# Optimization experiments

Hardware: AMD Instinct MI355X
Metric: run time of the kernel (lower is better)

## Reference

```python
import jax, jax.numpy as jnp
import numpy as np

N_NODES = 50000
N_EDGES = 1_600_000
D_IN = 128
D_HID = 128
D_OUT = 128


def _linear_init(key, out_dim, in_dim, bias=True):
    k1, k2 = jax.random.split(key)
    bound = 1.0 / np.sqrt(in_dim)
    W = jax.random.uniform(k1, (out_dim, in_dim), jnp.float32, -bound, bound)
    if bias:
        b = jax.random.uniform(k2, (out_dim,), jnp.float32, -bound, bound)
        return W, b
    return W, None


def _leconv_params(key, in_dim, out_dim):
    k1, k2, k3 = jax.random.split(key, 3)
    W1, b1 = _linear_init(k1, out_dim, in_dim, bias=True)   # lin1 (applied to x_j)
    W2, _ = _linear_init(k2, out_dim, in_dim, bias=False)   # lin2 (applied to x_i)
    W3, b3 = _linear_init(k3, out_dim, in_dim, bias=True)   # lin3 (skip on x_i)
    return W1, b1, W2, W3, b3


def setup_inputs() -> dict:
    key = jax.random.key(0)
    kx, ke, kw, k_in, k_mid, k_out = jax.random.split(key, 6)
    x = jax.random.normal(kx, (N_NODES, D_IN), jnp.float32)
    edge_index = jax.random.randint(ke, (2, N_EDGES), 0, N_NODES, dtype=jnp.int32)
    edge_weight = jax.random.uniform(kw, (N_EDGES,), jnp.float32)
    iW1, ib1, iW2, iW3, ib3 = _leconv_params(k_in, D_IN, D_HID)
    mW1, mb1, mW2, mW3, mb3 = _leconv_params(k_mid, D_HID, D_HID)
    oW1, ob1, oW2, oW3, ob3 = _leconv_params(k_out, D_HID, D_OUT)
    return {
        "x": x, "edge_index": edge_index, "edge_weight": edge_weight,
        "in_W1": iW1, "in_b1": ib1, "in_W2": iW2, "in_W3": iW3, "in_b3": ib3,
        "mid_W1": mW1, "mid_b1": mb1, "mid_W2": mW2, "mid_W3": mW3, "mid_b3": mb3,
        "out_W1": oW1, "out_b1": ob1, "out_W2": oW2, "out_W3": oW3, "out_b3": ob3,
        "number_of_layers": 4,
    }


def _leconv(h, src, dst, ew, W1, b1, W2, W3, b3):
    # out_i = sum_{j->i} e_ji * ((W1 x_j + b1) - W2 x_i) + (W3 x_i + b3)
    a = h @ W1.T + b1          # [N, F_out]
    b = h @ W2.T               # [N, F_out]
    msg = ew[:, None] * (a[src] - b[dst])              # [E, F_out]
    agg = jax.ops.segment_sum(msg, dst, num_segments=h.shape[0])
    return agg + h @ W3.T + b3


def _lrelu(x):
    return jnp.where(x >= 0, x, 0.1 * x)


def reference(x, edge_index, edge_weight,
              in_W1, in_b1, in_W2, in_W3, in_b3,
              mid_W1, mid_b1, mid_W2, mid_W3, mid_b3,
              out_W1, out_b1, out_W2, out_W3, out_b3,
              number_of_layers):
    src, dst = edge_index[0], edge_index[1]
    h = _lrelu(_leconv(x, src, dst, edge_weight, in_W1, in_b1, in_W2, in_W3, in_b3))
    for _ in range(number_of_layers - 2):  # shared inner weights, as in the torch module
        h = _lrelu(_leconv(h, src, dst, edge_weight, mid_W1, mid_b1, mid_W2, mid_W3, mid_b3))
    h = _lrelu(_leconv(h, src, dst, edge_weight, out_W1, out_b1, out_W2, out_W3, out_b3))
    return jax.nn.sigmoid(h)
```

## Files before the change

### kernel.cpp

```cpp
#include <hip/hip_runtime.h>
#include <hip/hip_fp16.h>
#include <math.h>

#define D 128
#define CSH 13
#define BSH 9
#define NB_MAX 128

typedef _Float16 f16;
typedef __attribute__((ext_vector_type(8))) _Float16 f16x8;
typedef __attribute__((ext_vector_type(4))) float f32x4;


__global__ __launch_bounds__(256) void binA_count(
    const int* __restrict__ dst, int* __restrict__ bucketCount, int E)
{
    __shared__ int hist[NB_MAX];
    int tid = threadIdx.x;
    if (tid < NB_MAX) hist[tid] = 0;
    __syncthreads();
    int base = blockIdx.x * 4096;
    for (int i = tid; i < 4096; i += 256) {
        int e = base + i;
        if (e < E) atomicAdd(&hist[dst[e] >> BSH], 1);
    }
    __syncthreads();
    if (tid < NB_MAX && hist[tid]) atomicAdd(&bucketCount[tid], hist[tid]);
}

__global__ void bucket_scan(
    const int* __restrict__ bucketCount, int* __restrict__ bucketBase,
    int* __restrict__ bucketCursor, int* __restrict__ row_off,
    int NBUC, int E, int N)
{
    if (threadIdx.x == 0 && blockIdx.x == 0) {
        int p = 0;
        for (int b = 0; b < NBUC; ++b) {
            bucketBase[b] = p; bucketCursor[b] = p; p += bucketCount[b];
        }
        bucketBase[NBUC] = p;
        row_off[N] = E;
    }
}

__global__ __launch_bounds__(256) void binA_scatter(
    const int* __restrict__ src, const int* __restrict__ dst,
    const float* __restrict__ ew, int* __restrict__ bucketCursor,
    int4* __restrict__ binned, int E)
{
    __shared__ int hist[NB_MAX], off[NB_MAX], cbase[NB_MAX];
    int tid = threadIdx.x;
    if (tid < NB_MAX) { hist[tid] = 0; off[tid] = 0; }
    __syncthreads();
    int base = blockIdx.x * 4096;
    for (int i = tid; i < 4096; i += 256) {
        int e = base + i;
        if (e < E) atomicAdd(&hist[dst[e] >> BSH], 1);
    }
    __syncthreads();
    if (tid < NB_MAX && hist[tid])
        cbase[tid] = atomicAdd(&bucketCursor[tid], hist[tid]);
    __syncthreads();
    for (int i = tid; i < 4096; i += 256) {
        int e = base + i;
        if (e < E) {
            int d = dst[e];
            int b = d >> BSH;
            int pos = cbase[b] + atomicAdd(&off[b], 1);
            binned[pos] = make_int4(src[e], __float_as_int(ew[e]), d, 0);
        }
    }
}

__global__ __launch_bounds__(1024) void binB_kernel(
    const int4* __restrict__ binned, const int* __restrict__ bucketBase,
    int2* __restrict__ edge_s, int* __restrict__ row_off,
    float* __restrict__ sdeg, int N, int nchunk)
{
    __shared__ int hist[4096];
    __shared__ int cur[4096];
    __shared__ float sdl[512];
    __shared__ int wsum[16];

    int b    = blockIdx.x;
    int tid  = threadIdx.x;
    int ebeg = bucketBase[b], eend = bucketBase[b + 1];
    int node0 = b << BSH;
    int nib   = min(512, N - node0);

    for (int i = tid; i < 4096; i += 1024) hist[i] = 0;
    for (int i = tid; i < 512; i += 1024) sdl[i] = 0.f;
    __syncthreads();

    for (int e = ebeg + tid; e < eend; e += 1024) {
        int4 ed = binned[e];
        int dl = ed.z - node0;
        int ch = ((unsigned)ed.x) >> CSH;
        atomicAdd(&hist[dl * nchunk + ch], 1);
        atomicAdd(&sdl[dl], __int_as_float(ed.y));
    }
    __syncthreads();

    int t4 = tid * 4;
    int h0 = hist[t4], h1 = hist[t4 + 1], h2 = hist[t4 + 2], h3 = hist[t4 + 3];
    int sum = h0 + h1 + h2 + h3;
    int lane = tid & 63, wid = tid >> 6;
    int x = sum;
    #pragma unroll
    for (int o = 1; o < 64; o <<= 1) { int t = __shfl_up(x, o); if (lane >= o) x += t; }
    if (lane == 63) wsum[wid] = x;
    __syncthreads();
    if (tid < 16) {
        int y = wsum[tid];
        #pragma unroll
        for (int o = 1; o < 16; o <<= 1) { int t = __shfl_up(y, o, 16); if (tid >= o) y += t; }
        wsum[tid] = y;
    }
    __syncthreads();
    int excl = (wid ? wsum[wid - 1] : 0) + x - sum;
    cur[t4] = excl; cur[t4 + 1] = excl + h0;
    cur[t4 + 2] = excl + h0 + h1; cur[t4 + 3] = excl + h0 + h1 + h2;
    __syncthreads();

    for (int dl = tid; dl < nib; dl += 1024) {
        row_off[node0 + dl] = ebeg + cur[dl * nchunk];
        sdeg[node0 + dl]    = sdl[dl];
    }
    __syncthreads();

    for (int e = ebeg + tid; e < eend; e += 1024) {
        int4 ed = binned[e];
        int dl = ed.z - node0;
        int ch = ((unsigned)ed.x) >> CSH;
        int pos = ebeg + atomicAdd(&cur[dl * nchunk + ch], 1);
        edge_s[pos] = make_int2(ed.x, ed.y);
    }
}

__global__ __launch_bounds__(256) void pack_kernel(
    const float* __restrict__ W1, const float* __restrict__ W2,
    const float* __restrict__ W3, f16* __restrict__ Wp)
{
    int idx = blockIdx.x * 256 + threadIdx.x;
    if (idx >= 6144) return;
    int lane = idx & 63;
    int t    = idx >> 6;
    int ks   = t & 3;
    int mot  = t >> 2;
    int m    = mot >> 3;
    int ot   = mot & 7;
    const float* W = (m == 0) ? W1 : (m == 1) ? W2 : W3;
    int o  = ot * 16 + (lane & 15);
    int kb = ks * 32 + (lane >> 4) * 8;
    f16x8 hi, lo;
    #pragma unroll
    for (int j = 0; j < 8; ++j) {
        float v = W[(size_t)o * D + kb + j];
        f16 hh = (f16)v;
        hi[j] = hh;
        lo[j] = (f16)(v - (float)hh);
    }
    size_t base = (size_t)ks * 24576 + (size_t)mot * 1024 + (size_t)lane * 8;
    *(f16x8*)&Wp[base]       = hi;
    *(f16x8*)&Wp[base + 512] = lo;
}

__global__ __launch_bounds__(256, 3) void gemm_kernel(
    const float* __restrict__ in, const f16* __restrict__ Wp,
    const float* __restrict__ b1, const float* __restrict__ b3,
    const float* __restrict__ sdeg, float* __restrict__ aA,
    float* __restrict__ aB, float* __restrict__ base_out, int N)
{
    __shared__ f16 Blds[24576];

    int tid  = threadIdx.x;
    int lane = tid & 63;
    int wid  = tid >> 6;
    int n0   = (blockIdx.x * 4 + wid) * 16;
    int col  = lane & 15;
    int g    = lane >> 4;
    int nrow = n0 + col;

    f32x4 acc[24];
    #pragma unroll
    for (int i = 0; i < 24; ++i) acc[i] = (f32x4){0.f, 0.f, 0.f, 0.f};

    for (int ks = 0; ks < 4; ++ks) {
        float av[8];
        if (nrow < N) {
            float4 a0 = *(const float4*)&in[(size_t)nrow * D + ks * 32 + g * 8];
            float4 a1 = *(const float4*)&in[(size_t)nrow * D + ks * 32 + g * 8 + 4];
            av[0] = a0.x; av[1] = a0.y; av[2] = a0.z; av[3] = a0.w;
            av[4] = a1.x; av[5] = a1.y; av[6] = a1.z; av[7] = a1.w;
        } else {
            #pragma unroll
            for (int j = 0; j < 8; ++j) av[j] = 0.f;
        }
        f16x8 ahi, alo;
        #pragma unroll
        for (int j = 0; j < 8; ++j) {
            f16 hh = (f16)av[j];
            ahi[j] = hh;
            alo[j] = (f16)(av[j] - (float)hh);
        }

        __syncthreads();
        {
            const f16x8* s4 = (const f16x8*)(Wp + (size_t)ks * 24576);
            f16x8* d4 = (f16x8*)Blds;
            for (int i = tid; i < 3072; i += 256) d4[i] = s4[i];
        }
        __syncthreads();

        #pragma unroll
        for (int mot = 0; mot < 24; ++mot) {
            f16x8 bhi = *(const f16x8*)&Blds[mot * 1024 + lane * 8];
            f16x8 blo = *(const f16x8*)&Blds[mot * 1024 + 512 + lane * 8];
            acc[mot] = __builtin_amdgcn_mfma_f32_16x16x32_f16(ahi, bhi, acc[mot], 0, 0, 0);
            acc[mot] = __builtin_amdgcn_mfma_f32_16x16x32_f16(alo, bhi, acc[mot], 0, 0, 0);
            acc[mot] = __builtin_amdgcn_mfma_f32_16x16x32_f16(ahi, blo, acc[mot], 0, 0, 0);
        }
    }

    #pragma unroll
    for (int ot = 0; ot < 8; ++ot) {
        int o = ot * 16 + col;
        float bi1 = b1[o];
        float bi3 = b3[o];
        float* ah = (o < 64) ? aA : aB;
        int    oh = o & 63;
        #pragma unroll
        for (int r = 0; r < 4; ++r) {
            int node = n0 + g * 4 + r;
            if (node < N) {
                float sv   = sdeg[node];
                float aval = acc[ot][r] + bi1;
                float bval = acc[16 + ot][r] + bi3 - sv * acc[8 + ot][r];
                ah[(size_t)node * 64 + oh]     = aval;
                base_out[(size_t)node * D + o] = bval;
            }
        }
    }
}


__global__ __launch_bounds__(256) void agg_kernel(
    const float* __restrict__ aH, const float* __restrict__ base,
    const int* __restrict__ row_off, const int2* __restrict__ edge_s,
    float* __restrict__ out, int N, int hofs, int last)
{
    int lane = threadIdx.x & 63;
    int node = blockIdx.x * 4 + (threadIdx.x >> 6);
    if (node >= N) return;

    float acc = base[(size_t)node * D + hofs + lane];
    int beg = row_off[node];
    int end = row_off[node + 1];

    int e = beg;
    if ((e & 1) && e < end) {
        int2 ed = edge_s[e];
        acc = fmaf(__int_as_float(ed.y), aH[(size_t)ed.x * 64 + lane], acc);
        ++e;
    }
    for (; e + 16 <= end; e += 16) {
        int4 ed[8];
        #pragma unroll
        for (int i = 0; i < 8; ++i) ed[i] = *(const int4*)&edge_s[e + i * 2];
        float v[16];
        #pragma unroll
        for (int i = 0; i < 8; ++i) {
            v[2 * i]     = aH[(size_t)ed[i].x * 64 + lane];
            v[2 * i + 1] = aH[(size_t)ed[i].z * 64 + lane];
        }
        #pragma unroll
        for (int i = 0; i < 8; ++i) {
            acc = fmaf(__int_as_float(ed[i].y), v[2 * i], acc);
            acc = fmaf(__int_as_float(ed[i].w), v[2 * i + 1], acc);
        }
    }
    for (; e + 4 <= end; e += 4) {
        int4 e0 = *(const int4*)&edge_s[e];
        int4 e1 = *(const int4*)&edge_s[e + 2];
        float v0 = aH[(size_t)e0.x * 64 + lane];
        float v1 = aH[(size_t)e0.z * 64 + lane];
        float v2 = aH[(size_t)e1.x * 64 + lane];
        float v3 = aH[(size_t)e1.z * 64 + lane];
        acc = fmaf(__int_as_float(e0.y), v0, acc);
        acc = fmaf(__int_as_float(e0.w), v1, acc);
        acc = fmaf(__int_as_float(e1.y), v2, acc);
        acc = fmaf(__int_as_float(e1.w), v3, acc);
    }
    for (; e < end; ++e) {
        int2 ed = edge_s[e];
        acc = fmaf(__int_as_float(ed.y), aH[(size_t)ed.x * 64 + lane], acc);
    }

    acc = acc >= 0.f ? acc : 0.1f * acc;
    if (last) acc = 1.f / (1.f + __expf(-acc));
    out[(size_t)node * D + hofs + lane] = acc;
}


extern "C" void kernel_launch(void* const* d_in, const int* in_sizes, int n_in,
                              void* d_out, int out_size, void* d_ws, size_t ws_size,
                              hipStream_t stream) {
    const float* x   = (const float*)d_in[0];
    const int*   ei  = (const int*)d_in[1];
    const float* ew  = (const float*)d_in[2];
    const float* iW1 = (const float*)d_in[3];
    const float* ib1 = (const float*)d_in[4];
    const float* iW2 = (const float*)d_in[5];
    const float* iW3 = (const float*)d_in[6];
    const float* ib3 = (const float*)d_in[7];
    const float* mW1 = (const float*)d_in[8];
    const float* mb1 = (const float*)d_in[9];
    const float* mW2 = (const float*)d_in[10];
    const float* mW3 = (const float*)d_in[11];
    const float* mb3 = (const float*)d_in[12];
    const float* oW1 = (const float*)d_in[13];
    const float* ob1 = (const float*)d_in[14];
    const float* oW2 = (const float*)d_in[15];
    const float* oW3 = (const float*)d_in[16];
    const float* ob3 = (const float*)d_in[17];

    int N = in_sizes[0] / D;
    int E = in_sizes[2];
    const int* src = ei;
    const int* dst = ei + E;
    int nchunk = (N + (1 << CSH) - 1) >> CSH;
    int NBUC   = (N + (1 << BSH) - 1) >> BSH;

    char* wsp = (char*)d_ws;
    size_t off = 0;
    auto alloc = [&](size_t bytes) -> void* {
        void* p = wsp + off;
        off += (bytes + 255) & ~(size_t)255;
        return p;
    };
    float* h        = (float*)alloc((size_t)N * D * 4);
    float* base     = (float*)alloc((size_t)N * D * 4);
    float* aA       = (float*)alloc((size_t)N * 64 * 4);
    float* aB       = (float*)alloc((size_t)N * 64 * 4);
    float* sdeg     = (float*)alloc((size_t)N * 4);
    int*   row_off  = (int*)alloc((size_t)(N + 1) * 4);
    int2*  edge_s   = (int2*)alloc((size_t)E * 8);
    int*   bucketCount  = (int*)alloc((size_t)(NBUC + 1) * 4);
    int*   bucketBase   = (int*)alloc((size_t)(NBUC + 1) * 4);
    int*   bucketCursor = (int*)alloc((size_t)(NBUC + 1) * 4);
    f16*   Wp       = (f16*)alloc((size_t)3 * 98304 * 2);

    int4* binned = (int4*)h;

    hipMemsetAsync(bucketCount, 0, (size_t)(NBUC + 1) * 4, stream);

    int ablocks  = (N + 3) / 4;
    int tiles    = (N + 15) / 16;
    int gblocks  = (tiles + 3) / 4;
    int abblocks = (E + 4095) / 4096;

    pack_kernel<<<24, 256, 0, stream>>>(iW1, iW2, iW3, Wp);
    pack_kernel<<<24, 256, 0, stream>>>(mW1, mW2, mW3, Wp + 98304);
    pack_kernel<<<24, 256, 0, stream>>>(oW1, oW2, oW3, Wp + 2 * 98304);

    binA_count<<<abblocks, 256, 0, stream>>>(dst, bucketCount, E);
    bucket_scan<<<1, 64, 0, stream>>>(bucketCount, bucketBase, bucketCursor,
                                      row_off, NBUC, E, N);
    binA_scatter<<<abblocks, 256, 0, stream>>>(src, dst, ew, bucketCursor,
                                               binned, E);
    binB_kernel<<<NBUC, 1024, 0, stream>>>(binned, bucketBase, edge_s,
                                           row_off, sdeg, N, nchunk);

    gemm_kernel<<<gblocks, 256, 0, stream>>>(x, Wp, ib1, ib3, sdeg, aA, aB, base, N);
    agg_kernel<<<ablocks, 256, 0, stream>>>(aA, base, row_off, edge_s, h, N, 0, 0);
    agg_kernel<<<ablocks, 256, 0, stream>>>(aB, base, row_off, edge_s, h, N, 64, 0);
    for (int l = 0; l < 2; ++l) {
        gemm_kernel<<<gblocks, 256, 0, stream>>>(h, Wp + 98304, mb1, mb3, sdeg, aA, aB, base, N);
        agg_kernel<<<ablocks, 256, 0, stream>>>(aA, base, row_off, edge_s, h, N, 0, 0);
        agg_kernel<<<ablocks, 256, 0, stream>>>(aB, base, row_off, edge_s, h, N, 64, 0);
    }
    gemm_kernel<<<gblocks, 256, 0, stream>>>(h, Wp + 2 * 98304, ob1, ob3, sdeg, aA, aB, base, N);
    agg_kernel<<<ablocks, 256, 0, stream>>>(aA, base, row_off, edge_s, (float*)d_out, N, 0, 1);
    agg_kernel<<<ablocks, 256, 0, stream>>>(aB, base, row_off, edge_s, (float*)d_out, N, 64, 1);
}
```

Measured before the change: 727.3 us.

## Make GEMM persistent with register-resident weights and merge agg halves into one launch

The GEMM kernel now runs a fixed grid of persistent blocks, and each wave keeps its slice of the packed split-f16 weights in registers. This replaces re-staging the full weight matrix through LDS for every 64-row block. Each block processes 16-row tiles, with its four waves splitting the output columns. The two aggregation launches per layer are combined into one kernel in which paired waves handle the two 64-column halves of the same node. The register-resident weights raise VGPR pressure and lower occupancy, and each input tile is now read by four waves.

Measured after the change: 679.9 us. 6.5% less time.

```diff
diff --git a/kernel.cpp b/kernel.cpp
--- a/kernel.cpp
+++ b/kernel.cpp
@@ -165,93 +165,115 @@
     *(f16x8*)&Wp[base + 512] = lo;
 }
 
-__global__ __launch_bounds__(256, 3) void gemm_kernel(
+
+__global__ __launch_bounds__(256, 2) void gemm_kernel(
     const float* __restrict__ in, const f16* __restrict__ Wp,
     const float* __restrict__ b1, const float* __restrict__ b3,
     const float* __restrict__ sdeg, float* __restrict__ aA,
-    float* __restrict__ aB, float* __restrict__ base_out, int N)
-{
-    __shared__ f16 Blds[24576];
-
+    float* __restrict__ aB, float* __restrict__ base_out,
+    int N, int ntiles, int gridb)
+{
     int tid  = threadIdx.x;
     int lane = tid & 63;
     int wid  = tid >> 6;
-    int n0   = (blockIdx.x * 4 + wid) * 16;
     int col  = lane & 15;
     int g    = lane >> 4;
-    int nrow = n0 + col;
-
-    f32x4 acc[24];
+
+    f16x8 w[3][2][4][2];
     #pragma unroll
-    for (int i = 0; i < 24; ++i) acc[i] = (f32x4){0.f, 0.f, 0.f, 0.f};
-
-    for (int ks = 0; ks < 4; ++ks) {
-        float av[8];
-        if (nrow < N) {
-            float4 a0 = *(const float4*)&in[(size_t)nrow * D + ks * 32 + g * 8];
-            float4 a1 = *(const float4*)&in[(size_t)nrow * D + ks * 32 + g * 8 + 4];
-            av[0] = a0.x; av[1] = a0.y; av[2] = a0.z; av[3] = a0.w;
-            av[4] = a1.x; av[5] = a1.y; av[6] = a1.z; av[7] = a1.w;
-        } else {
+    for (int m = 0; m < 3; ++m)
+        #pragma unroll
+        for (int oti = 0; oti < 2; ++oti) {
+            int mot = m * 8 + wid * 2 + oti;
             #pragma unroll
-            for (int j = 0; j < 8; ++j) av[j] = 0.f;
-        }
-        f16x8 ahi, alo;
-        #pragma unroll
-        for (int j = 0; j < 8; ++j) {
-            f16 hh = (f16)av[j];
-            ahi[j] = hh;
-            alo[j] = (f16)(av[j] - (float)hh);
-        }
-
-        __syncthreads();
-        {
-            const f16x8* s4 = (const f16x8*)(Wp + (size_t)ks * 24576);
-            f16x8* d4 = (f16x8*)Blds;
-            for (int i = tid; i < 3072; i += 256) d4[i] = s4[i];
-        }
-        __syncthreads();
-
-        #pragma unroll
-        for (int mot = 0; mot < 24; ++mot) {
-            f16x8 bhi = *(const f16x8*)&Blds[mot * 1024 + lane * 8];
-            f16x8 blo = *(const f16x8*)&Blds[mot * 1024 + 512 + lane * 8];
-            acc[mot] = __builtin_amdgcn_mfma_f32_16x16x32_f16(ahi, bhi, acc[mot], 0, 0, 0);
-            acc[mot] = __builtin_amdgcn_mfma_f32_16x16x32_f16(alo, bhi, acc[mot], 0, 0, 0);
-            acc[mot] = __builtin_amdgcn_mfma_f32_16x16x32_f16(ahi, blo, acc[mot], 0, 0, 0);
-        }
-    }
-
+            for (int ks = 0; ks < 4; ++ks) {
+                const f16* p = Wp + (size_t)ks * 24576 + (size_t)mot * 1024 + (size_t)lane * 8;
+                w[m][oti][ks][0] = *(const f16x8*)p;
+                w[m][oti][ks][1] = *(const f16x8*)(p + 512);
+            }
+        }
+
+    float bi1[2], bi3[2];
     #pragma unroll
-    for (int ot = 0; ot < 8; ++ot) {
-        int o = ot * 16 + col;
-        float bi1 = b1[o];
-        float bi3 = b3[o];
-        float* ah = (o < 64) ? aA : aB;
-        int    oh = o & 63;
-        #pragma unroll
-        for (int r = 0; r < 4; ++r) {
-            int node = n0 + g * 4 + r;
-            if (node < N) {
-                float sv   = sdeg[node];
-                float aval = acc[ot][r] + bi1;
-                float bval = acc[16 + ot][r] + bi3 - sv * acc[8 + ot][r];
-                ah[(size_t)node * 64 + oh]     = aval;
-                base_out[(size_t)node * D + o] = bval;
+    for (int oti = 0; oti < 2; ++oti) {
+        int o = (wid * 2 + oti) * 16 + col;
+        bi1[oti] = b1[o];
+        bi3[oti] = b3[o];
+    }
+
+    for (int t = blockIdx.x; t < ntiles; t += gridb) {
+        int n0   = t * 16;
+        int nrow = n0 + col;
+
+        f32x4 acc[3][2];
+        #pragma unroll
+        for (int m = 0; m < 3; ++m)
+            #pragma unroll
+            for (int oti = 0; oti < 2; ++oti)
+                acc[m][oti] = (f32x4){0.f, 0.f, 0.f, 0.f};
+
+        #pragma unroll
+        for (int ks = 0; ks < 4; ++ks) {
+            float av[8];
+            if (nrow < N) {
+                float4 a0 = *(const float4*)&in[(size_t)nrow * D + ks * 32 + g * 8];
+                float4 a1 = *(const float4*)&in[(size_t)nrow * D + ks * 32 + g * 8 + 4];
+                av[0] = a0.x; av[1] = a0.y; av[2] = a0.z; av[3] = a0.w;
+                av[4] = a1.x; av[5] = a1.y; av[6] = a1.z; av[7] = a1.w;
+            } else {
+                #pragma unroll
+                for (int j = 0; j < 8; ++j) av[j] = 0.f;
             }
+            f16x8 ahi, alo;
+            #pragma unroll
+            for (int j = 0; j < 8; ++j) {
+                f16 hh = (f16)av[j];
+                ahi[j] = hh;
+                alo[j] = (f16)(av[j] - (float)hh);
+            }
+            #pragma unroll
+            for (int m = 0; m < 3; ++m)
+                #pragma unroll
+                for (int oti = 0; oti < 2; ++oti) {
+                    acc[m][oti] = __builtin_amdgcn_mfma_f32_16x16x32_f16(ahi, w[m][oti][ks][0], acc[m][oti], 0, 0, 0);
+                    acc[m][oti] = __builtin_amdgcn_mfma_f32_16x16x32_f16(alo, w[m][oti][ks][0], acc[m][oti], 0, 0, 0);
+                    acc[m][oti] = __builtin_amdgcn_mfma_f32_16x16x32_f16(ahi, w[m][oti][ks][1], acc[m][oti], 0, 0, 0);
+                }
+        }
+
+        float* ah = (wid < 2) ? aA : aB;
+        #pragma unroll
+        for (int oti = 0; oti < 2; ++oti) {
+            int o  = (wid * 2 + oti) * 16 + col;
+            int oh = o & 63;
+            #pragma unroll
+            for (int r = 0; r < 4; ++r) {
+                int node = n0 + g * 4 + r;
+                if (node < N) {
+                    float sv   = sdeg[node];
+                    float aval = acc[0][oti][r] + bi1[oti];
+                    float bval = acc[2][oti][r] + bi3[oti] - sv * acc[1][oti][r];
+                    ah[(size_t)node * 64 + oh]     = aval;
+                    base_out[(size_t)node * D + o] = bval;
+                }
+            }
         }
     }
 }
 
 
 __global__ __launch_bounds__(256) void agg_kernel(
-    const float* __restrict__ aH, const float* __restrict__ base,
-    const int* __restrict__ row_off, const int2* __restrict__ edge_s,
-    float* __restrict__ out, int N, int hofs, int last)
+    const float* __restrict__ aA, const float* __restrict__ aB,
+    const float* __restrict__ base, const int* __restrict__ row_off,
+    const int2* __restrict__ edge_s, float* __restrict__ out, int N, int last)
 {
     int lane = threadIdx.x & 63;
-    int node = blockIdx.x * 4 + (threadIdx.x >> 6);
+    int wid  = threadIdx.x >> 6;
+    int node = blockIdx.x * 2 + (wid >> 1);
+    int half = wid & 1;
     if (node >= N) return;
+    const float* aH = half ? aB : aA;
+    int hofs = half << 6;
 
     float acc = base[(size_t)node * D + hofs + lane];
     int beg = row_off[node];
@@ -354,10 +376,10 @@
 
     hipMemsetAsync(bucketCount, 0, (size_t)(NBUC + 1) * 4, stream);
 
-    int ablocks  = (N + 3) / 4;
-    int tiles    = (N + 15) / 16;
-    int gblocks  = (tiles + 3) / 4;
-    int abblocks = (E + 4095) / 4096;
+    int aggblocks = (N + 1) / 2;
+    int ntiles    = (N + 15) / 16;
+    int gridb     = 512;
+    int abblocks  = (E + 4095) / 4096;
 
     pack_kernel<<<24, 256, 0, stream>>>(iW1, iW2, iW3, Wp);
     pack_kernel<<<24, 256, 0, stream>>>(mW1, mW2, mW3, Wp + 98304);
@@ -371,15 +393,12 @@
     binB_kernel<<<NBUC, 1024, 0, stream>>>(binned, bucketBase, edge_s,
                                            row_off, sdeg, N, nchunk);
 
-    gemm_kernel<<<gblocks, 256, 0, stream>>>(x, Wp, ib1, ib3, sdeg, aA, aB, base, N);
-    agg_kernel<<<ablocks, 256, 0, stream>>>(aA, base, row_off, edge_s, h, N, 0, 0);
-    agg_kernel<<<ablocks, 256, 0, stream>>>(aB, base, row_off, edge_s, h, N, 64, 0);
+    gemm_kernel<<<gridb, 256, 0, stream>>>(x, Wp, ib1, ib3, sdeg, aA, aB, base, N, ntiles, gridb);
+    agg_kernel<<<aggblocks, 256, 0, stream>>>(aA, aB, base, row_off, edge_s, h, N, 0);
     for (int l = 0; l < 2; ++l) {
-        gemm_kernel<<<gblocks, 256, 0, stream>>>(h, Wp + 98304, mb1, mb3, sdeg, aA, aB, base, N);
-        agg_kernel<<<ablocks, 256, 0, stream>>>(aA, base, row_off, edge_s, h, N, 0, 0);
-        agg_kernel<<<ablocks, 256, 0, stream>>>(aB, base, row_off, edge_s, h, N, 64, 0);
-    }
-    gemm_kernel<<<gblocks, 256, 0, stream>>>(h, Wp + 2 * 98304, ob1, ob3, sdeg, aA, aB, base, N);
-    agg_kernel<<<ablocks, 256, 0, stream>>>(aA, base, row_off, edge_s, (float*)d_out, N, 0, 1);
-    agg_kernel<<<ablocks, 256, 0, stream>>>(aB, base, row_off, edge_s, (float*)d_out, N, 64, 1);
-}
+        gemm_kernel<<<gridb, 256, 0, stream>>>(h, Wp + 98304, mb1, mb3, sdeg, aA, aB, base, N, ntiles, gridb);
+        agg_kernel<<<aggblocks, 256, 0, stream>>>(aA, aB, base, row_off, edge_s, h, N, 0);
+    }
+    gemm_kernel<<<gridb, 256, 0, stream>>>(h, Wp + 2 * 98304, ob1, ob3, sdeg, aA, aB, base, N, ntiles, gridb);
+    agg_kernel<<<aggblocks, 256, 0, stream>>>(aA, aB, base, row_off, edge_s, (float*)d_out, N, 1);
+}
```
